# Kernel optimization log

Measured on AMD Instinct MI355X. Metric: run time of the kernel, lower is better.

## Reference

```python
import jax, jax.numpy as jnp
import numpy as np

COMMITMENT_COST = 0.25
N_EMBED = 1024
EMB_DIM = 256

def setup_inputs() -> dict:
    key = jax.random.key(0)
    k1, k2 = jax.random.split(key)
    z = jax.random.normal(k1, (32, EMB_DIM, 32, 32), dtype=jnp.float32)
    # embedding.weight.data.uniform_(-1/n_embed, 1/n_embed)
    embedding = jax.random.uniform(k2, (N_EMBED, EMB_DIM), dtype=jnp.float32,
                                   minval=-1.0 / N_EMBED, maxval=1.0 / N_EMBED)
    return {"z": z, "embedding": embedding}

def reference(z, embedding):
    # NCHW -> NHWC
    zp = jnp.transpose(z, (0, 2, 3, 1))            # [B,H,W,D]
    in_shape = zp.shape
    flat = zp.reshape(-1, in_shape[-1])            # [N,D]
    # squared L2 distances (argmin equivalent to p=2 cdist argmin)
    d2 = (jnp.sum(flat * flat, axis=1, keepdims=True)
          - 2.0 * (flat @ embedding.T)
          + jnp.sum(embedding * embedding, axis=1))  # [N,K]
    idx = jnp.argmin(d2, axis=1)                   # [N]
    # one-hot @ codebook == direct gather
    z_quant = embedding[idx].reshape(in_shape)     # [B,H,W,D]
    codebook_loss = jnp.mean((z_quant - jax.lax.stop_gradient(zp)) ** 2)
    commitment_loss = jnp.mean((zp - jax.lax.stop_gradient(z_quant)) ** 2)
    loss = codebook_loss + COMMITMENT_COST * commitment_loss
    # straight-through estimator
    z_st = zp + jax.lax.stop_gradient(z_quant - zp)
    z_st = jnp.transpose(z_st, (0, 3, 1, 2))       # NHWC -> NCHW
    return (z_st, loss, codebook_loss, commitment_loss)
```

## Files before the change

kernel.cpp:

```cpp
#include <hip/hip_runtime.h>
#include <hip/hip_bf16.h>
#include <stdint.h>


typedef short v8s __attribute__((ext_vector_type(8)));
typedef float v4f __attribute__((ext_vector_type(4)));

__device__ inline unsigned short f2bf(float f) {
    uint32_t u = __float_as_uint(f);
    return (unsigned short)((u + 0x7fffu + ((u >> 16) & 1u)) >> 16);
}

__global__ __launch_bounds__(256) void k_prep_e(const float* __restrict__ E,
                                                v8s* __restrict__ Esw,
                                                float* __restrict__ nE,
                                                float* __restrict__ accum,
                                                unsigned* __restrict__ done) {
    __shared__ float Ef[16][264];
    int q = blockIdx.x, tid = threadIdx.x;
    const float4* Ein = (const float4*)(E + ((size_t)q << 12));
#pragma unroll
    for (int i = 0; i < 4; i++) {
        int f4 = i * 256 + tid;
        int row = f4 >> 6, c4 = (f4 & 63) << 2;
        *(float4*)&Ef[row][c4] = Ein[f4];
    }
    __syncthreads();
    {
        int c = tid >> 4, l = tid & 15;
        float s = 0.f;
#pragma unroll
        for (int j = 0; j < 16; j++) { float v = Ef[c][l + 16 * j]; s += v * v; }
#pragma unroll
        for (int off = 1; off < 16; off <<= 1) s += __shfl_xor(s, off);
        if (l == 0) nE[q * 16 + c] = 0.5f * s;
    }
#pragma unroll
    for (int i = 0; i < 2; i++) {
        int u = tid + i * 256;
        int um = u & 15, ug = (u >> 4) & 3, udc = (u >> 6) & 7;
        int d0 = udc * 32 + ug * 8;
        union { v8s v; unsigned short s[8]; } pk;
#pragma unroll
        for (int e = 0; e < 8; e++) pk.s[e] = f2bf(Ef[um][d0 + e]);
        Esw[((size_t)q << 9) + u] = pk.v;
    }
    if (q == 0 && tid == 0) { accum[0] = 0.f; done[0] = 0u; }
}

__global__ __launch_bounds__(512) void k_main(
        const v8s* __restrict__ Esw,
        const float* __restrict__ nE,
        const float* __restrict__ z,
        const float* __restrict__ E,
        float* __restrict__ out,
        float* __restrict__ accum,
        unsigned* __restrict__ done) {
    __shared__ union {
        v8s    B[2][4096];
        float4 Eg4[2048];
    } S;
    __shared__ float nEl[1024];
    __shared__ float nrmLds[128];
    __shared__ int   idxLds[128];
    __shared__ float w8[8];

    int tid = threadIdx.x;
    int lane = tid & 63, w = tid >> 6;
    int g = lane >> 4, m = lane & 15;
    int R0 = blockIdx.x << 7;
    int b = R0 >> 10, hw0 = R0 & 1023;

    {
        int q = tid & 31, dblk = tid >> 5;
        const float* zp = z + ((size_t)b << 18) + hw0 + (q << 2);
#pragma unroll
        for (int s = 0; s < 2; s++) {
            float4 L[8];
#pragma unroll
            for (int j = 0; j < 8; j++)
                L[j] = *(const float4*)(zp + (size_t)(((dblk << 4) + (s << 3) + j) << 10));
            const float* Lf = (const float*)L;
            int slot = (dblk << 1) + s;
#pragma unroll
            for (int c = 0; c < 4; c++) {
                union { v8s v; unsigned short u[8]; } pk;
#pragma unroll
                for (int j = 0; j < 8; j++) pk.u[j] = f2bf(Lf[j * 4 + c]);
                int row = (q << 2) + c;
                int sw = slot ^ ((row ^ (row >> 2)) & 7);
                *(v8s*)((char*)&S + (row << 9) + (sw << 4)) = pk.v;
            }
        }
    }
#pragma unroll
    for (int i = 0; i < 2; i++) nEl[tid + i * 512] = nE[tid + i * 512];
    __syncthreads();

    v8s a[8];
    {
        int row = (w << 4) + m;
        int f = (row ^ (row >> 2)) & 7;
#pragma unroll
        for (int dc = 0; dc < 8; dc++) {
            int sw = ((dc << 2) + g) ^ f;
            a[dc] = *(const v8s*)((const char*)&S + (row << 9) + (sw << 4));
        }
        float nrm = 0.f;
#pragma unroll
        for (int dc = 0; dc < 8; dc++) {
            union { v8s v; unsigned short u[8]; } un; un.v = a[dc];
#pragma unroll
            for (int j = 0; j < 8; j++) {
                float v = __uint_as_float((uint32_t)un.u[j] << 16);
                nrm = fmaf(v, v, nrm);
            }
        }
        nrm += __shfl_xor(nrm, 16);
        nrm += __shfl_xor(nrm, 32);
        if (g == 0) nrmLds[row] = nrm;
    }
    __syncthreads();

#define STAGE(ch, buf)                                                        \
    {                                                                         \
        _Pragma("unroll")                                                     \
        for (int j = 0; j < 8; j++) {                                         \
            __builtin_amdgcn_global_load_lds(                                 \
                (const __attribute__((address_space(1))) void*)               \
                    (Esw + ((size_t)(ch) << 12) + (j << 9) + (w << 6) + lane),\
                (__attribute__((address_space(3))) void*)                     \
                    &S.B[buf][(j << 9) + (w << 6)],                           \
                16, 0, 0);                                                    \
        }                                                                     \
    }

    float best[4]; int bidx[4];
#pragma unroll
    for (int r = 0; r < 4; r++) { best[r] = 3.4e38f; bidx[r] = 0; }

    STAGE(0, 0);
#pragma unroll 2
    for (int ct = 0; ct < 8; ct++) {
        int cur = ct & 1;
        __syncthreads();
        if (ct < 7) STAGE(ct + 1, cur ^ 1);
        float ne[8];
#pragma unroll
        for (int t = 0; t < 8; t++) ne[t] = nEl[(ct << 7) + (t << 4) + m];
        v4f acc[8];
#pragma unroll
        for (int t = 0; t < 8; t++) acc[t] = (v4f){0.f, 0.f, 0.f, 0.f};
#pragma unroll
        for (int dc = 0; dc < 8; dc++) {
#pragma unroll
            for (int t = 0; t < 8; t++) {
                v8s bf = S.B[cur][t * 512 + dc * 64 + g * 16 + m];
                acc[t] = __builtin_amdgcn_mfma_f32_16x16x32_bf16(a[dc], bf, acc[t], 0, 0, 0);
            }
        }
#pragma unroll
        for (int t = 0; t < 8; t++) {
            int code = (ct << 7) + (t << 4) + m;
#pragma unroll
            for (int r = 0; r < 4; r++) {
                float s0 = ne[t] - acc[t][r];
                if (s0 < best[r]) { best[r] = s0; bidx[r] = code; }
            }
        }
    }

    float lsum = 0.f;
#pragma unroll
    for (int r = 0; r < 4; r++) {
        uint32_t sb = __float_as_uint(best[r]);
        sb = (sb & 0x80000000u) ? ~sb : (sb | 0x80000000u);
        unsigned long long pk = ((unsigned long long)sb << 32) | (uint32_t)bidx[r];
#pragma unroll
        for (int off = 1; off < 16; off <<= 1) {
            unsigned long long o = __shfl_xor(pk, off);
            if (o < pk) pk = o;
        }
        int row = (w << 4) + (g << 2) + r;
        if (m == 0) {
            idxLds[row] = (int)(pk & 0xffffffffu);
            uint32_t t = (uint32_t)(pk >> 32);
            float sw = __uint_as_float((t & 0x80000000u) ? (t & 0x7fffffffu) : ~t);
            lsum += 2.0f * sw + nrmLds[row];
        }
    }
#pragma unroll
    for (int off = 1; off < 64; off <<= 1) lsum += __shfl_xor(lsum, off);
    if (lane == 0) w8[w] = lsum;
    __syncthreads();

    float* ob = out + ((size_t)b << 18);
    int hwl = tid & 31, dq0 = tid >> 5;
#pragma unroll 1
    for (int ph = 0; ph < 4; ph++) {
#pragma unroll
        for (int i = 0; i < 4; i++) {
            int row = w + (i << 3);
            int k = idxLds[(ph << 5) + row];
            float4 v = ((const float4*)(E + ((size_t)k << 8)))[lane];
            S.Eg4[(row << 6) + (lane ^ row)] = v;
        }
        __syncthreads();
        int hwp = hw0 + (ph << 5) + hwl;
#pragma unroll
        for (int i = 0; i < 4; i++) {
            int dq = dq0 + (i << 4);
            float4 ev = S.Eg4[(hwl << 6) + (dq ^ hwl)];
            size_t o = ((size_t)dq << 12) + hwp;
            ob[o] = ev.x; ob[o + 1024] = ev.y; ob[o + 2048] = ev.z; ob[o + 3072] = ev.w;
        }
        __syncthreads();
    }

    if (tid == 0) {
        float s8 = 0.f;
#pragma unroll
        for (int i = 0; i < 8; i++) s8 += w8[i];
        atomicAdd(accum, s8);
        __threadfence();
        unsigned old = atomicAdd(done, 1u);
        if (old == 255u) {
            float s = atomicAdd(accum, 0.f) * (1.0f / 8388608.0f);
            out[8388608] = 1.25f * s;
            out[8388609] = s;
            out[8388610] = s;
        }
    }
#undef STAGE
}

extern "C" void kernel_launch(void* const* d_in, const int* in_sizes, int n_in,
                              void* d_out, int out_size, void* d_ws, size_t ws_size,
                              hipStream_t stream) {
    const float* z = (const float*)d_in[0];
    const float* E = (const float*)d_in[1];
    char* ws = (char*)d_ws;
    v8s*      Esw   = (v8s*)(ws);
    float*    nE    = (float*)(ws + 524288);
    float*    accum = (float*)(ws + 528384);
    unsigned* done  = (unsigned*)(ws + 528388);
    float* out = (float*)d_out;

    hipLaunchKernelGGL(k_prep_e, dim3(64),  dim3(256), 0, stream, E, Esw, nE, accum, done);
    hipLaunchKernelGGL(k_main,   dim3(256), dim3(512), 0, stream,
                       Esw, nE, z, E, out, accum, done);
}
```

Baseline: 116.9 us.

## Split codebook across wave halves with two row tiles per wave

```diff
diff --git a/kernel.cpp b/kernel.cpp
--- a/kernel.cpp
+++ b/kernel.cpp
@@ -48,7 +48,7 @@
     if (q == 0 && tid == 0) { accum[0] = 0.f; done[0] = 0u; }
 }
 
-__global__ __launch_bounds__(512) void k_main(
+__global__ __launch_bounds__(512, 2) void k_main(
         const v8s* __restrict__ Esw,
         const float* __restrict__ nE,
         const float* __restrict__ z,
@@ -61,13 +61,15 @@
         float4 Eg4[2048];
     } S;
     __shared__ float nEl[1024];
+    __shared__ unsigned long long pairLds[128][2];
     __shared__ float nrmLds[128];
     __shared__ int   idxLds[128];
-    __shared__ float w8[8];
+    __shared__ float w8[2];
 
     int tid = threadIdx.x;
     int lane = tid & 63, w = tid >> 6;
     int g = lane >> 4, m = lane & 15;
+    int rg = w & 3, h = w >> 2;
     int R0 = blockIdx.x << 7;
     int b = R0 >> 10, hw0 = R0 & 1023;
 
@@ -97,28 +99,35 @@
     for (int i = 0; i < 2; i++) nEl[tid + i * 512] = nE[tid + i * 512];
     __syncthreads();
 
-    v8s a[8];
+    v8s a0[8], a1[8];
     {
-        int row = (w << 4) + m;
-        int f = (row ^ (row >> 2)) & 7;
+        int row0 = (rg << 5) + m;
+        int row1 = row0 + 16;
+        int f0 = (row0 ^ (row0 >> 2)) & 7;
+        int f1 = (row1 ^ (row1 >> 2)) & 7;
 #pragma unroll
         for (int dc = 0; dc < 8; dc++) {
-            int sw = ((dc << 2) + g) ^ f;
-            a[dc] = *(const v8s*)((const char*)&S + (row << 9) + (sw << 4));
-        }
-        float nrm = 0.f;
-#pragma unroll
-        for (int dc = 0; dc < 8; dc++) {
-            union { v8s v; unsigned short u[8]; } un; un.v = a[dc];
-#pragma unroll
-            for (int j = 0; j < 8; j++) {
-                float v = __uint_as_float((uint32_t)un.u[j] << 16);
-                nrm = fmaf(v, v, nrm);
-            }
-        }
-        nrm += __shfl_xor(nrm, 16);
-        nrm += __shfl_xor(nrm, 32);
-        if (g == 0) nrmLds[row] = nrm;
+            a0[dc] = *(const v8s*)((const char*)&S + (row0 << 9) + ((((dc << 2) + g) ^ f0) << 4));
+            a1[dc] = *(const v8s*)((const char*)&S + (row1 << 9) + ((((dc << 2) + g) ^ f1) << 4));
+        }
+        if (h == 0) {
+            float n0 = 0.f, n1 = 0.f;
+#pragma unroll
+            for (int dc = 0; dc < 8; dc++) {
+                union { v8s v; unsigned short u[8]; } u0, u1;
+                u0.v = a0[dc]; u1.v = a1[dc];
+#pragma unroll
+                for (int j = 0; j < 8; j++) {
+                    float v0 = __uint_as_float((uint32_t)u0.u[j] << 16);
+                    float v1 = __uint_as_float((uint32_t)u1.u[j] << 16);
+                    n0 = fmaf(v0, v0, n0);
+                    n1 = fmaf(v1, v1, n1);
+                }
+            }
+            n0 += __shfl_xor(n0, 16); n0 += __shfl_xor(n0, 32);
+            n1 += __shfl_xor(n1, 16); n1 += __shfl_xor(n1, 32);
+            if (g == 0) { nrmLds[row0] = n0; nrmLds[row1] = n1; }
+        }
     }
     __syncthreads();
 
@@ -135,9 +144,12 @@
         }                                                                     \
     }
 
-    float best[4]; int bidx[4];
-#pragma unroll
-    for (int r = 0; r < 4; r++) { best[r] = 3.4e38f; bidx[r] = 0; }
+    float best0[4], best1[4]; int bidx0[4], bidx1[4];
+#pragma unroll
+    for (int r = 0; r < 4; r++) {
+        best0[r] = 3.4e38f; bidx0[r] = 0;
+        best1[r] = 3.4e38f; bidx1[r] = 0;
+    }
 
     STAGE(0, 0);
 #pragma unroll 2
@@ -145,53 +157,70 @@
         int cur = ct & 1;
         __syncthreads();
         if (ct < 7) STAGE(ct + 1, cur ^ 1);
-        float ne[8];
-#pragma unroll
-        for (int t = 0; t < 8; t++) ne[t] = nEl[(ct << 7) + (t << 4) + m];
-        v4f acc[8];
-#pragma unroll
-        for (int t = 0; t < 8; t++) acc[t] = (v4f){0.f, 0.f, 0.f, 0.f};
+        float ne[4];
+#pragma unroll
+        for (int t = 0; t < 4; t++) ne[t] = nEl[(ct << 7) + (h << 6) + (t << 4) + m];
+        v4f acc0[4], acc1[4];
+#pragma unroll
+        for (int t = 0; t < 4; t++) {
+            acc0[t] = (v4f){0.f, 0.f, 0.f, 0.f};
+            acc1[t] = (v4f){0.f, 0.f, 0.f, 0.f};
+        }
 #pragma unroll
         for (int dc = 0; dc < 8; dc++) {
 #pragma unroll
-            for (int t = 0; t < 8; t++) {
-                v8s bf = S.B[cur][t * 512 + dc * 64 + g * 16 + m];
-                acc[t] = __builtin_amdgcn_mfma_f32_16x16x32_bf16(a[dc], bf, acc[t], 0, 0, 0);
-            }
-        }
-#pragma unroll
-        for (int t = 0; t < 8; t++) {
-            int code = (ct << 7) + (t << 4) + m;
+            for (int t = 0; t < 4; t++) {
+                v8s bf = S.B[cur][((h << 2) + t) * 512 + dc * 64 + g * 16 + m];
+                acc0[t] = __builtin_amdgcn_mfma_f32_16x16x32_bf16(a0[dc], bf, acc0[t], 0, 0, 0);
+                acc1[t] = __builtin_amdgcn_mfma_f32_16x16x32_bf16(a1[dc], bf, acc1[t], 0, 0, 0);
+            }
+        }
+#pragma unroll
+        for (int t = 0; t < 4; t++) {
+            int code = (ct << 7) + (h << 6) + (t << 4) + m;
 #pragma unroll
             for (int r = 0; r < 4; r++) {
-                float s0 = ne[t] - acc[t][r];
-                if (s0 < best[r]) { best[r] = s0; bidx[r] = code; }
-            }
-        }
-    }
-
-    float lsum = 0.f;
+                float s0 = ne[t] - acc0[t][r];
+                if (s0 < best0[r]) { best0[r] = s0; bidx0[r] = code; }
+                float s1 = ne[t] - acc1[t][r];
+                if (s1 < best1[r]) { best1[r] = s1; bidx1[r] = code; }
+            }
+        }
+    }
+
 #pragma unroll
     for (int r = 0; r < 4; r++) {
-        uint32_t sb = __float_as_uint(best[r]);
-        sb = (sb & 0x80000000u) ? ~sb : (sb | 0x80000000u);
-        unsigned long long pk = ((unsigned long long)sb << 32) | (uint32_t)bidx[r];
+        uint32_t sb0 = __float_as_uint(best0[r]);
+        sb0 = (sb0 & 0x80000000u) ? ~sb0 : (sb0 | 0x80000000u);
+        unsigned long long pk0 = ((unsigned long long)sb0 << 32) | (uint32_t)bidx0[r];
+        uint32_t sb1 = __float_as_uint(best1[r]);
+        sb1 = (sb1 & 0x80000000u) ? ~sb1 : (sb1 | 0x80000000u);
+        unsigned long long pk1 = ((unsigned long long)sb1 << 32) | (uint32_t)bidx1[r];
 #pragma unroll
         for (int off = 1; off < 16; off <<= 1) {
-            unsigned long long o = __shfl_xor(pk, off);
-            if (o < pk) pk = o;
-        }
-        int row = (w << 4) + (g << 2) + r;
+            unsigned long long o0 = __shfl_xor(pk0, off);
+            if (o0 < pk0) pk0 = o0;
+            unsigned long long o1 = __shfl_xor(pk1, off);
+            if (o1 < pk1) pk1 = o1;
+        }
         if (m == 0) {
-            idxLds[row] = (int)(pk & 0xffffffffu);
-            uint32_t t = (uint32_t)(pk >> 32);
-            float sw = __uint_as_float((t & 0x80000000u) ? (t & 0x7fffffffu) : ~t);
-            lsum += 2.0f * sw + nrmLds[row];
-        }
-    }
-#pragma unroll
-    for (int off = 1; off < 64; off <<= 1) lsum += __shfl_xor(lsum, off);
-    if (lane == 0) w8[w] = lsum;
+            pairLds[(rg << 5) + (g << 2) + r][h] = pk0;
+            pairLds[(rg << 5) + 16 + (g << 2) + r][h] = pk1;
+        }
+    }
+    __syncthreads();
+
+    if (tid < 128) {
+        unsigned long long p0 = pairLds[tid][0], p1 = pairLds[tid][1];
+        unsigned long long pk = p1 < p0 ? p1 : p0;
+        idxLds[tid] = (int)(pk & 0xffffffffu);
+        uint32_t t = (uint32_t)(pk >> 32);
+        float sc = __uint_as_float((t & 0x80000000u) ? (t & 0x7fffffffu) : ~t);
+        float ls = 2.0f * sc + nrmLds[tid];
+#pragma unroll
+        for (int off = 1; off < 64; off <<= 1) ls += __shfl_xor(ls, off);
+        if (lane == 0) w8[w] = ls;
+    }
     __syncthreads();
 
     float* ob = out + ((size_t)b << 18);
@@ -218,10 +247,7 @@
     }
 
     if (tid == 0) {
-        float s8 = 0.f;
-#pragma unroll
-        for (int i = 0; i < 8; i++) s8 += w8[i];
-        atomicAdd(accum, s8);
+        atomicAdd(accum, w8[0] + w8[1]);
         __threadfence();
         unsigned old = atomicAdd(done, 1u);
         if (old == 255u) {
```

New measurement: 118.0 us. Within noise of the previous version (+0.9%).

## Deepen codebook staging to a four-buffer pipeline with explicit vmcnt waits

Applied to the files above, without the earlier changes.

```diff
diff --git a/kernel.cpp b/kernel.cpp
--- a/kernel.cpp
+++ b/kernel.cpp
@@ -57,7 +57,7 @@
         float* __restrict__ accum,
         unsigned* __restrict__ done) {
     __shared__ union {
-        v8s    B[2][4096];
+        v8s    B[4][2048];
         float4 Eg4[2048];
     } S;
     __shared__ float nEl[1024];
@@ -125,10 +125,10 @@
 #define STAGE(ch, buf)                                                        \
     {                                                                         \
         _Pragma("unroll")                                                     \
-        for (int j = 0; j < 8; j++) {                                         \
+        for (int j = 0; j < 4; j++) {                                         \
             __builtin_amdgcn_global_load_lds(                                 \
                 (const __attribute__((address_space(1))) void*)               \
-                    (Esw + ((size_t)(ch) << 12) + (j << 9) + (w << 6) + lane),\
+                    (Esw + ((size_t)(ch) << 11) + (j << 9) + (w << 6) + lane),\
                 (__attribute__((address_space(3))) void*)                     \
                     &S.B[buf][(j << 9) + (w << 6)],                           \
                 16, 0, 0);                                                    \
@@ -139,36 +139,44 @@
 #pragma unroll
     for (int r = 0; r < 4; r++) { best[r] = 3.4e38f; bidx[r] = 0; }
 
-    STAGE(0, 0);
-#pragma unroll 2
-    for (int ct = 0; ct < 8; ct++) {
-        int cur = ct & 1;
-        __syncthreads();
-        if (ct < 7) STAGE(ct + 1, cur ^ 1);
-        float ne[8];
-#pragma unroll
-        for (int t = 0; t < 8; t++) ne[t] = nEl[(ct << 7) + (t << 4) + m];
-        v4f acc[8];
-#pragma unroll
-        for (int t = 0; t < 8; t++) acc[t] = (v4f){0.f, 0.f, 0.f, 0.f};
-#pragma unroll
-        for (int dc = 0; dc < 8; dc++) {
-#pragma unroll
-            for (int t = 0; t < 8; t++) {
-                v8s bf = S.B[cur][t * 512 + dc * 64 + g * 16 + m];
-                acc[t] = __builtin_amdgcn_mfma_f32_16x16x32_bf16(a[dc], bf, acc[t], 0, 0, 0);
-            }
-        }
-#pragma unroll
-        for (int t = 0; t < 8; t++) {
-            int code = (ct << 7) + (t << 4) + m;
-#pragma unroll
-            for (int r = 0; r < 4; r++) {
-                float s0 = ne[t] - acc[t][r];
-                if (s0 < best[r]) { best[r] = s0; bidx[r] = code; }
-            }
-        }
-    }
+#define CHUNK(CT, NW)                                                         \
+    {                                                                         \
+        asm volatile("s_waitcnt vmcnt(" #NW ")" ::: "memory");                \
+        __builtin_amdgcn_s_barrier();                                         \
+        float ne_[4];                                                         \
+        _Pragma("unroll")                                                     \
+        for (int t = 0; t < 4; t++) ne_[t] = nEl[((CT) << 6) + t * 16 + m];   \
+        v4f acc_[4];                                                          \
+        _Pragma("unroll")                                                     \
+        for (int t = 0; t < 4; t++) acc_[t] = (v4f){0.f, 0.f, 0.f, 0.f};      \
+        _Pragma("unroll")                                                     \
+        for (int dc = 0; dc < 8; dc++) {                                      \
+            _Pragma("unroll")                                                 \
+            for (int t = 0; t < 4; t++) {                                     \
+                v8s bf = S.B[(CT) & 3][t * 512 + dc * 64 + g * 16 + m];       \
+                acc_[t] = __builtin_amdgcn_mfma_f32_16x16x32_bf16(            \
+                              a[dc], bf, acc_[t], 0, 0, 0);                   \
+            }                                                                 \
+        }                                                                     \
+        _Pragma("unroll")                                                     \
+        for (int t = 0; t < 4; t++) {                                         \
+            int code = ((CT) << 6) + t * 16 + m;                              \
+            _Pragma("unroll")                                                 \
+            for (int r = 0; r < 4; r++) {                                     \
+                float s0 = ne_[t] - acc_[t][r];                               \
+                if (s0 < best[r]) { best[r] = s0; bidx[r] = code; }           \
+            }                                                                 \
+        }                                                                     \
+        asm volatile("s_waitcnt lgkmcnt(0)" ::: "memory");                    \
+        __builtin_amdgcn_s_barrier();                                         \
+        if ((CT) < 12) STAGE((CT) + 4, (CT) & 3);                             \
+    }
+
+    STAGE(0, 0); STAGE(1, 1); STAGE(2, 2); STAGE(3, 3);
+    CHUNK(0, 12)  CHUNK(1, 12)  CHUNK(2, 12)  CHUNK(3, 12)
+    CHUNK(4, 12)  CHUNK(5, 12)  CHUNK(6, 12)  CHUNK(7, 12)
+    CHUNK(8, 12)  CHUNK(9, 12)  CHUNK(10, 12) CHUNK(11, 12)
+    CHUNK(12, 12) CHUNK(13, 8)  CHUNK(14, 4)  CHUNK(15, 0)
 
     float lsum = 0.f;
 #pragma unroll
@@ -231,6 +239,7 @@
             out[8388610] = s;
         }
     }
+#undef CHUNK
 #undef STAGE
 }
 
```

After: 118.5 us. No clear change (+1.3%).

## Split codebook gather and NCHW writeback into a separate wide epilogue kernel

Applied to the files above, without the earlier changes.

```diff
diff --git a/kernel.cpp b/kernel.cpp
--- a/kernel.cpp
+++ b/kernel.cpp
@@ -14,8 +14,7 @@
 __global__ __launch_bounds__(256) void k_prep_e(const float* __restrict__ E,
                                                 v8s* __restrict__ Esw,
                                                 float* __restrict__ nE,
-                                                float* __restrict__ accum,
-                                                unsigned* __restrict__ done) {
+                                                float* __restrict__ accum) {
     __shared__ float Ef[16][264];
     int q = blockIdx.x, tid = threadIdx.x;
     const float4* Ein = (const float4*)(E + ((size_t)q << 12));
@@ -45,24 +44,20 @@
         for (int e = 0; e < 8; e++) pk.s[e] = f2bf(Ef[um][d0 + e]);
         Esw[((size_t)q << 9) + u] = pk.v;
     }
-    if (q == 0 && tid == 0) { accum[0] = 0.f; done[0] = 0u; }
+    if (q == 0 && tid == 0) accum[0] = 0.f;
 }
 
 __global__ __launch_bounds__(512) void k_main(
         const v8s* __restrict__ Esw,
         const float* __restrict__ nE,
         const float* __restrict__ z,
-        const float* __restrict__ E,
-        float* __restrict__ out,
-        float* __restrict__ accum,
-        unsigned* __restrict__ done) {
+        int* __restrict__ idxG,
+        float* __restrict__ accum) {
     __shared__ union {
-        v8s    B[2][4096];
-        float4 Eg4[2048];
+        v8s B[2][4096];
     } S;
     __shared__ float nEl[1024];
     __shared__ float nrmLds[128];
-    __shared__ int   idxLds[128];
     __shared__ float w8[8];
 
     int tid = threadIdx.x;
@@ -183,7 +178,7 @@
         }
         int row = (w << 4) + (g << 2) + r;
         if (m == 0) {
-            idxLds[row] = (int)(pk & 0xffffffffu);
+            idxG[R0 + row] = (int)(pk & 0xffffffffu);
             uint32_t t = (uint32_t)(pk >> 32);
             float sw = __uint_as_float((t & 0x80000000u) ? (t & 0x7fffffffu) : ~t);
             lsum += 2.0f * sw + nrmLds[row];
@@ -193,45 +188,40 @@
     for (int off = 1; off < 64; off <<= 1) lsum += __shfl_xor(lsum, off);
     if (lane == 0) w8[w] = lsum;
     __syncthreads();
-
-    float* ob = out + ((size_t)b << 18);
-    int hwl = tid & 31, dq0 = tid >> 5;
-#pragma unroll 1
-    for (int ph = 0; ph < 4; ph++) {
-#pragma unroll
-        for (int i = 0; i < 4; i++) {
-            int row = w + (i << 3);
-            int k = idxLds[(ph << 5) + row];
-            float4 v = ((const float4*)(E + ((size_t)k << 8)))[lane];
-            S.Eg4[(row << 6) + (lane ^ row)] = v;
-        }
-        __syncthreads();
-        int hwp = hw0 + (ph << 5) + hwl;
-#pragma unroll
-        for (int i = 0; i < 4; i++) {
-            int dq = dq0 + (i << 4);
-            float4 ev = S.Eg4[(hwl << 6) + (dq ^ hwl)];
-            size_t o = ((size_t)dq << 12) + hwp;
-            ob[o] = ev.x; ob[o + 1024] = ev.y; ob[o + 2048] = ev.z; ob[o + 3072] = ev.w;
-        }
-        __syncthreads();
-    }
-
     if (tid == 0) {
         float s8 = 0.f;
 #pragma unroll
         for (int i = 0; i < 8; i++) s8 += w8[i];
         atomicAdd(accum, s8);
-        __threadfence();
-        unsigned old = atomicAdd(done, 1u);
-        if (old == 255u) {
-            float s = atomicAdd(accum, 0.f) * (1.0f / 8388608.0f);
-            out[8388608] = 1.25f * s;
-            out[8388609] = s;
-            out[8388610] = s;
-        }
     }
 #undef STAGE
+}
+
+__global__ __launch_bounds__(256) void k_epi(const int* __restrict__ idxG,
+                                             const float* __restrict__ E,
+                                             const float* __restrict__ accum,
+                                             float* __restrict__ out) {
+    int j = blockIdx.x, t = threadIdx.x;
+    int b = j >> 6, d0 = (j & 63) << 2;
+    int4 kk = ((const int4*)(idxG + (b << 10)))[t];
+    float4 e0 = *(const float4*)(E + ((size_t)kk.x << 8) + d0);
+    float4 e1 = *(const float4*)(E + ((size_t)kk.y << 8) + d0);
+    float4 e2 = *(const float4*)(E + ((size_t)kk.z << 8) + d0);
+    float4 e3 = *(const float4*)(E + ((size_t)kk.w << 8) + d0);
+    const float* p0 = &e0.x; const float* p1 = &e1.x;
+    const float* p2 = &e2.x; const float* p3 = &e3.x;
+    float* ob = out + ((size_t)b << 18) + ((size_t)d0 << 10) + (t << 2);
+#pragma unroll
+    for (int i = 0; i < 4; i++) {
+        float4 v; v.x = p0[i]; v.y = p1[i]; v.z = p2[i]; v.w = p3[i];
+        *(float4*)(ob + (size_t)i * 1024) = v;
+    }
+    if (j == 0 && t == 0) {
+        float s = atomicAdd((float*)accum, 0.f) * (1.0f / 8388608.0f);
+        out[8388608] = 1.25f * s;
+        out[8388609] = s;
+        out[8388610] = s;
+    }
 }
 
 extern "C" void kernel_launch(void* const* d_in, const int* in_sizes, int n_in,
@@ -240,13 +230,15 @@
     const float* z = (const float*)d_in[0];
     const float* E = (const float*)d_in[1];
     char* ws = (char*)d_ws;
-    v8s*      Esw   = (v8s*)(ws);
-    float*    nE    = (float*)(ws + 524288);
-    float*    accum = (float*)(ws + 528384);
-    unsigned* done  = (unsigned*)(ws + 528388);
+    v8s*   Esw   = (v8s*)(ws);
+    float* nE    = (float*)(ws + 524288);
+    float* accum = (float*)(ws + 528384);
+    int*   idxG  = (int*)(ws + 532480);
     float* out = (float*)d_out;
 
-    hipLaunchKernelGGL(k_prep_e, dim3(64),  dim3(256), 0, stream, E, Esw, nE, accum, done);
-    hipLaunchKernelGGL(k_main,   dim3(256), dim3(512), 0, stream,
-                       Esw, nE, z, E, out, accum, done);
-}
+    hipLaunchKernelGGL(k_prep_e, dim3(64),   dim3(256), 0, stream, E, Esw, nE, accum);
+    hipLaunchKernelGGL(k_main,   dim3(256),  dim3(512), 0, stream,
+                       Esw, nE, z, idxG, accum);
+    hipLaunchKernelGGL(k_epi,    dim3(2048), dim3(256), 0, stream,
+                       idxG, E, accum, out);
+}
```

After: 116.2 us. No clear change (-0.7%).
